# Kernel tuning notes

Measured on AMD Instinct MI355X. Metric: run time of the kernel, lower is better.

The kernel has to match this reference:

```python
import jax, jax.numpy as jnp
import numpy as np

UNITS = 1024
N_FEATURES = 128
OUT_STEPS = 32
EPS = 1e-7


def _lstm_cell(x, h, c, W, U, b):
    # Keras LSTMCell: gates ordered i, f, g(candidate), o
    z = x @ W + h @ U + b  # [B, 4U]
    i, f, g, o = jnp.split(z, 4, axis=-1)
    i = jax.nn.sigmoid(i)
    f = jax.nn.sigmoid(f)
    g = jnp.tanh(g)
    o = jax.nn.sigmoid(o)
    c_new = f * c + i * g
    h_new = o * jnp.tanh(c_new)
    return h_new, c_new


def setup_inputs() -> dict:
    key = jax.random.key(0)
    ks = jax.random.split(key, 12)
    B, T, F, U = 512, 64, N_FEATURES, UNITS
    s = lambda fan_in: 1.0 / np.sqrt(fan_in)
    return {
        "inputs": jax.random.normal(ks[0], (B, T, F), jnp.float32),
        "mean": jax.random.normal(ks[1], (F,), jnp.float32) * 0.1,
        "var": jax.random.uniform(ks[2], (F,), jnp.float32, 0.5, 1.5),
        "W1": jax.random.normal(ks[3], (F, 4 * U), jnp.float32) * s(F),
        "U1": jax.random.normal(ks[4], (U, 4 * U), jnp.float32) * s(U),
        "b1": jnp.zeros((4 * U,), jnp.float32),
        "W2": jax.random.normal(ks[5], (U, 4 * U), jnp.float32) * s(U),
        "U2": jax.random.normal(ks[6], (U, 4 * U), jnp.float32) * s(U),
        "b2": jnp.zeros((4 * U,), jnp.float32),
        "Wd": jax.random.normal(ks[7], (U, F), jnp.float32) * s(U),
        "bd": jnp.zeros((F,), jnp.float32),
    }


def reference(inputs, mean, var, W1, U1, b1, W2, U2, b2, Wd, bd):
    B = inputs.shape[0]
    inv_std = jax.lax.rsqrt(var + EPS)
    # NOTE: original call() normalizes, then warmup() normalizes AGAIN -- faithful.
    x = (inputs - mean) * inv_std
    x = (x - mean) * inv_std

    # --- warmup: RNN(cell1) over input sequence, return last h and state ---
    h0 = jnp.zeros((B, UNITS), x.dtype)
    c0 = jnp.zeros((B, UNITS), x.dtype)

    def warm_step(carry, xt):
        h, c = carry
        h, c = _lstm_cell(xt, h, c, W1, U1, b1)
        return (h, c), None

    (h, c), _ = jax.lax.scan(warm_step, (h0, c0), jnp.swapaxes(x, 0, 1))
    pred0 = h @ Wd + bd  # [B, F]

    def ar_step(carry, _):
        pred, h, c = carry
        h, c = _lstm_cell(pred, h, c, W1, U1, b1)
        h, c = _lstm_cell(h, h, c, W2, U2, b2)
        pred = h @ Wd + bd
        return (pred, h, c), pred

    _, preds = jax.lax.scan(ar_step, (pred0, h, c), None, length=OUT_STEPS - 1)
    preds = jnp.concatenate([pred0[None], preds], axis=0)  # [out_steps, B, F]
    return jnp.transpose(preds, (1, 0, 2))  # [B, out_steps, F]
```

## Files before the change

kernel.cpp:

```cpp
#include <hip/hip_runtime.h>
#include <stdint.h>

#define NB 512
#define NT 64
#define NF 128
#define NU 1024
#define NG 4096
#define NS 32

typedef __attribute__((ext_vector_type(8))) short short8;
typedef __attribute__((ext_vector_type(4))) float f32x4;
typedef __attribute__((ext_vector_type(16))) float f32x16;
typedef __attribute__((ext_vector_type(4))) unsigned int u32x4;

__device__ __forceinline__ float sigm(float x) { return 1.0f / (1.0f + __expf(-x)); }
__device__ __forceinline__ float tanh_f(float x) {
  float ax = fabsf(x);
  float e = __expf(2.0f * ax);
  float t = 1.0f - 2.0f / (e + 1.0f);
  return copysignf(t, x);
}
__device__ __forceinline__ unsigned short f2bf(float f) {
  union { float f; unsigned u; } v; v.f = f;
  unsigned r = v.u + 0x7fffu + ((v.u >> 16) & 1u);
  return (unsigned short)(r >> 16);
}

__device__ __forceinline__ void coh_store_bf16(unsigned short* p, unsigned v) {
  asm volatile("global_store_short %0, %1, off sc0 sc1" :: "v"(p), "v"(v) : "memory");
}

__device__ __forceinline__ void gbar_grp(unsigned* gf, int u_blk, unsigned gen) {
  __syncthreads();
  if (threadIdx.x == 0)
    __hip_atomic_store(gf + u_blk, gen, __ATOMIC_RELAXED, __HIP_MEMORY_SCOPE_AGENT);
  if (threadIdx.x < 32) {
    while (__hip_atomic_load(gf + threadIdx.x, __ATOMIC_RELAXED, __HIP_MEMORY_SCOPE_AGENT) < gen)
      __builtin_amdgcn_s_sleep(1);
  }
  __syncthreads();
}

template <int KX>
__device__ __forceinline__ void do_step(
    const unsigned short* __restrict__ hIn,
    const unsigned short* __restrict__ Bp,
    const unsigned short* __restrict__ Xp,
    const unsigned short* __restrict__ W1p,
    int tstep, f32x4 bA, f32x4& cst,
    unsigned short* __restrict__ hOut, unsigned short* __restrict__ hOut2,
    unsigned short* lds,
    int r0, int u0, int kh, int g, int tid)
{
  constexpr int ROWB = (NU + KX) * 2;
  const int lane = tid & 63;
  const int lu = lane & 31;
  const int lk = lane >> 5;

  {
    u32x4 ta[8], tb[8];
    int la[8], lb[8];
#pragma unroll
    for (int it = 0; it < 8; ++it) {
      int i = tid + it * 512;
      int r = i >> 7, cb = i & 127;
      la[it] = r * ROWB + ((cb * 16) ^ ((r & 7) << 4));
      const unsigned short* gp = hIn + (size_t)(r0 + r) * NU + cb * 8;
      asm volatile("global_load_dwordx4 %0, %1, off sc0 sc1" : "=v"(ta[it]) : "v"(gp));
    }
#pragma unroll
    for (int it = 0; it < 8; ++it) {
      int i = tid + (8 + it) * 512;
      int r = i >> 7, cb = i & 127;
      lb[it] = r * ROWB + ((cb * 16) ^ ((r & 7) << 4));
      const unsigned short* gp = hIn + (size_t)(r0 + r) * NU + cb * 8;
      asm volatile("global_load_dwordx4 %0, %1, off sc0 sc1" : "=v"(tb[it]) : "v"(gp));
    }
    if constexpr (KX > 0) {
      u32x4 tx[2]; int ox[2];
#pragma unroll
      for (int it = 0; it < 2; ++it) {
        int i = tid + it * 512;
        int r = i >> 4, cb = i & 15;
        ox[it] = r * ROWB + ((NU * 2 + cb * 16) ^ ((r & 7) << 4));
        const unsigned short* gp = Xp + ((size_t)tstep * NB + (r0 + r)) * NF + cb * 8;
        asm volatile("global_load_dwordx4 %0, %1, off" : "=v"(tx[it]) : "v"(gp));
      }
      asm volatile("s_waitcnt vmcnt(10)" ::: "memory");
      __builtin_amdgcn_sched_barrier(0);
#pragma unroll
      for (int it = 0; it < 8; ++it) *(u32x4*)((char*)lds + la[it]) = ta[it];
      asm volatile("s_waitcnt vmcnt(2)" ::: "memory");
      __builtin_amdgcn_sched_barrier(0);
#pragma unroll
      for (int it = 0; it < 8; ++it) *(u32x4*)((char*)lds + lb[it]) = tb[it];
      asm volatile("s_waitcnt vmcnt(0)" ::: "memory");
      __builtin_amdgcn_sched_barrier(0);
#pragma unroll
      for (int it = 0; it < 2; ++it) *(u32x4*)((char*)lds + ox[it]) = tx[it];
    } else {
      asm volatile("s_waitcnt vmcnt(8)" ::: "memory");
      __builtin_amdgcn_sched_barrier(0);
#pragma unroll
      for (int it = 0; it < 8; ++it) *(u32x4*)((char*)lds + la[it]) = ta[it];
      asm volatile("s_waitcnt vmcnt(0)" ::: "memory");
      __builtin_amdgcn_sched_barrier(0);
#pragma unroll
      for (int it = 0; it < 8; ++it) *(u32x4*)((char*)lds + lb[it]) = tb[it];
    }
  }
  __syncthreads();

  f32x16 acc0 = (f32x16)0.0f;
  f32x16 acc1 = (f32x16)0.0f;

  const char* ldsb = (const char*)lds;
  const int axor = (lane & 7) << 4;
  const int arow0 = lu * ROWB;
  const int arow1 = (32 + lu) * ROWB;
  const int kbase = kh * 1024;
  const size_t cB = (size_t)g * NU + u0 + lu;

  short8 nb0 = *(const short8*)(Bp + ((size_t)(kh * 64 + 0 + lk) * NG + cB) * 8);
  short8 nb1 = *(const short8*)(Bp + ((size_t)(kh * 64 + 2 + lk) * NG + cB) * 8);
#pragma unroll 4
  for (int kc = 0; kc < 32; ++kc) {
    short8 bb = (kc & 1) ? nb1 : nb0;
    if (kc < 30) {
      short8 nv = *(const short8*)(Bp + ((size_t)(kh * 64 + (kc + 2) * 2 + lk) * NG + cB) * 8);
      if (kc & 1) nb1 = nv; else nb0 = nv;
    }
    int kb = (kbase + kc * 32 + lk * 16) ^ axor;
    short8 a0 = *(const short8*)(ldsb + arow0 + kb);
    short8 a1 = *(const short8*)(ldsb + arow1 + kb);
    acc0 = __builtin_amdgcn_mfma_f32_32x32x16_bf16(a0, bb, acc0, 0, 0, 0);
    acc1 = __builtin_amdgcn_mfma_f32_32x32x16_bf16(a1, bb, acc1, 0, 0, 0);
  }
  if constexpr (KX > 0) {
#pragma unroll
    for (int kx = 0; kx < 4; ++kx) {
      short8 bb = *(const short8*)(W1p + ((size_t)(kh * 8 + kx * 2 + lk) * NG + cB) * 8);
      int kb = (NU * 2 + kh * 128 + kx * 32 + lk * 16) ^ axor;
      short8 a0 = *(const short8*)(ldsb + arow0 + kb);
      short8 a1 = *(const short8*)(ldsb + arow1 + kb);
      acc0 = __builtin_amdgcn_mfma_f32_32x32x16_bf16(a0, bb, acc0, 0, 0, 0);
      acc1 = __builtin_amdgcn_mfma_f32_32x32x16_bf16(a1, bb, acc1, 0, 0, 0);
    }
  }

  __syncthreads();
  float* ex = (float*)lds;
  const int w8 = kh * 4 + g;
#pragma unroll
  for (int e = 0; e < 16; ++e) {
    ex[(w8 * 2 + 0) * 1024 + e * 64 + lane] = acc0[e];
    ex[(w8 * 2 + 1) * 1024 + e * 64 + lane] = acc1[e];
  }
  __syncthreads();

  const int u = tid & 31;
  const int rb = (tid >> 5) << 2;
  const int rh = tid >> 8;
  const int c4 = (tid >> 6) & 3;
  const int lane_src = (((tid >> 5) & 1) << 5) | u;
  f32x4 z[4];
#pragma unroll
  for (int gg = 0; gg < 4; ++gg) {
#pragma unroll
    for (int j = 0; j < 4; ++j) {
      int e = c4 * 4 + j;
      z[gg][j] = ex[((0 + gg) * 2 + rh) * 1024 + e * 64 + lane_src]
               + ex[((4 + gg) * 2 + rh) * 1024 + e * 64 + lane_src];
    }
  }
#pragma unroll
  for (int j = 0; j < 4; ++j) {
    size_t idx = (size_t)(r0 + rb + j) * NU + (u0 + u);
    float iv = sigm(z[0][j] + bA[0]);
    float fv = sigm(z[1][j] + bA[1]);
    float gv = tanh_f(z[2][j] + bA[2]);
    float ov = sigm(z[3][j] + bA[3]);
    float cN = fv * cst[j] + iv * gv;
    cst[j] = cN;
    unsigned hv = f2bf(ov * tanh_f(cN));
    coh_store_bf16(hOut + idx, hv);
    if (hOut2) coh_store_bf16(hOut2 + idx, hv);
  }
}

__global__ __launch_bounds__(512, 1) void lstm_seq(
    const unsigned short* __restrict__ U1p, const unsigned short* __restrict__ U1pp,
    const unsigned short* __restrict__ W2U2p, const unsigned short* __restrict__ W1p,
    const unsigned short* __restrict__ x2,
    const float* __restrict__ b1, const float* __restrict__ b1p, const float* __restrict__ b2,
    unsigned short* __restrict__ h0, unsigned short* __restrict__ h1,
    unsigned short* __restrict__ hist, unsigned* __restrict__ flags)
{
  extern __shared__ unsigned short lds[];
  const int bid = blockIdx.x;
  const int xcd = bid & 7, slot = bid >> 3;
  const int u_blk = xcd * 4 + (slot >> 3);
  const int m_blk = slot & 7;
  const int r0 = m_blk * 64, u0 = u_blk * 32;
  const int tid = threadIdx.x;
  const int w = tid >> 6, kh = w >> 2, g = w & 3;
  const size_t HS = (size_t)NB * NU;
  unsigned* gf = flags + m_blk * 64;

  const int ub = u0 + (tid & 31);
  f32x4 bW, bC1, bC2;
#pragma unroll
  for (int gg = 0; gg < 4; ++gg) {
    bW[gg]  = b1 [gg * NU + ub];
    bC1[gg] = b1p[gg * NU + ub];
    bC2[gg] = b2 [gg * NU + ub];
  }
  f32x4 cst = (f32x4){0.f, 0.f, 0.f, 0.f};

  unsigned gen = 0;
  for (int t = 0; t < NT; ++t) {
    const unsigned short* hi = (t & 1) ? h1 : h0;
    unsigned short* ho = (t & 1) ? h0 : h1;
    do_step<NF>(hi, U1p, x2, W1p, t, bW, cst, ho, (t == NT - 1) ? hist : nullptr,
                lds, r0, u0, kh, g, tid);
    gbar_grp(gf, u_blk, ++gen);
  }
  for (int s = 0; s < NS - 1; ++s) {
    do_step<0>(h0, U1pp, nullptr, nullptr, 0, bC1, cst, h1, nullptr,
               lds, r0, u0, kh, g, tid);
    gbar_grp(gf, u_blk, ++gen);
    do_step<0>(h1, W2U2p, nullptr, nullptr, 0, bC2, cst, h0, hist + (size_t)(s + 1) * HS,
               lds, r0, u0, kh, g, tid);
    gbar_grp(gf, u_blk, ++gen);
  }
}

__global__ __launch_bounds__(256, 2) void pred_gemm(
    const unsigned short* __restrict__ H,
    const unsigned short* __restrict__ Wdp,
    const float* __restrict__ bd, float* __restrict__ out)
{
  __shared__ unsigned short lds[32 * NU];
  const int tid = threadIdx.x;
  const int r0 = blockIdx.x * 32;
  for (int i = tid; i < 32 * 128; i += 256) {
    int r = i >> 7, cb = i & 127;
    uint4 v = *(const uint4*)(H + (size_t)(r0 + r) * NU + cb * 8);
    int off = r * 2048 + ((cb * 16) ^ ((r & 7) << 4));
    *(uint4*)((char*)lds + off) = v;
  }
  __syncthreads();
  const int w = tid >> 6, l = tid & 63, lr = l & 15, g4 = l >> 4;
  f32x4 acc[2][2];
#pragma unroll
  for (int a = 0; a < 2; ++a)
#pragma unroll
    for (int c = 0; c < 2; ++c) acc[a][c] = (f32x4){0.f, 0.f, 0.f, 0.f};
  const char* ldsb = (const char*)lds;
  const int arow0 = lr * 2048, arow1 = (16 + lr) * 2048, axor = (lr & 7) << 4;
  const int col0 = w * 32 + lr;
#pragma unroll 4
  for (int kc = 0; kc < 32; ++kc) {
    int kb = (kc * 64 + g4 * 16) ^ axor;
    short8 a0 = *(const short8*)(ldsb + arow0 + kb);
    short8 a1 = *(const short8*)(ldsb + arow1 + kb);
    size_t base = ((size_t)(kc * 4 + g4) * NF) * 8;
    short8 w0 = *(const short8*)(Wdp + base + (size_t)col0 * 8);
    short8 w1 = *(const short8*)(Wdp + base + (size_t)(col0 + 16) * 8);
    acc[0][0] = __builtin_amdgcn_mfma_f32_16x16x32_bf16(a0, w0, acc[0][0], 0, 0, 0);
    acc[1][0] = __builtin_amdgcn_mfma_f32_16x16x32_bf16(a1, w0, acc[1][0], 0, 0, 0);
    acc[0][1] = __builtin_amdgcn_mfma_f32_16x16x32_bf16(a0, w1, acc[0][1], 0, 0, 0);
    acc[1][1] = __builtin_amdgcn_mfma_f32_16x16x32_bf16(a1, w1, acc[1][1], 0, 0, 0);
  }
#pragma unroll
  for (int rt = 0; rt < 2; ++rt)
#pragma unroll
    for (int ct = 0; ct < 2; ++ct)
#pragma unroll
      for (int j = 0; j < 4; ++j) {
        int r = r0 + rt * 16 + g4 * 4 + j;
        int s = r >> 9, bb = r & 511;
        int f = w * 32 + ct * 16 + lr;
        out[((size_t)bb * NS + s) * NF + f] = acc[rt][ct][j] + bd[f];
      }
}

__global__ void prep_x(const float* __restrict__ in, const float* __restrict__ mean,
                       const float* __restrict__ var, unsigned short* __restrict__ x2) {
  int i = (blockIdx.x * 256 + threadIdx.x) * 4;
  int f = i & 127;
  int bt = i >> 7;
  int b = bt >> 6, t = bt & 63;
  float4 v = *(const float4*)(in + i);
  float vv[4] = {v.x, v.y, v.z, v.w};
  unsigned short o[4] __attribute__((aligned(8)));
#pragma unroll
  for (int j = 0; j < 4; ++j) {
    float inv = rsqrtf(var[f + j] + 1e-7f);
    float s = inv * inv;
    float m2 = mean[f + j] * (s + inv);
    o[j] = f2bf(vv[j] * s - m2);
  }
  *(uint2*)(x2 + (((size_t)t * NB + b) << 7) + f) = *(const uint2*)o;
}

__global__ void prep_pack(const float* __restrict__ A, const float* __restrict__ A2,
                          unsigned short* __restrict__ P, int N) {
  int idx = blockIdx.x * 256 + threadIdx.x;
  int kg = idx / N, c = idx - kg * N;
  unsigned short o[8] __attribute__((aligned(16)));
#pragma unroll
  for (int j = 0; j < 8; ++j) {
    size_t e = (size_t)(kg * 8 + j) * N + c;
    float vv = A[e];
    if (A2) vv += A2[e];
    o[j] = f2bf(vv);
  }
  *(uint4*)(P + (size_t)idx * 8) = *(const uint4*)o;
}

__global__ __launch_bounds__(256) void prep_u1pp(
    const float* __restrict__ U1, const float* __restrict__ Wd,
    const float* __restrict__ W1, unsigned short* __restrict__ P) {
  __shared__ float wd[8][NF];
  const int kg = blockIdx.x >> 4;
  const int c = ((blockIdx.x & 15) << 8) + threadIdx.x;
  for (int i = threadIdx.x; i < 8 * NF; i += 256)
    wd[i >> 7][i & 127] = Wd[(size_t)(kg * 8 + (i >> 7)) * NF + (i & 127)];
  __syncthreads();
  float a[8];
#pragma unroll
  for (int j = 0; j < 8; ++j) a[j] = U1[(size_t)(kg * 8 + j) * NG + c];
#pragma unroll 8
  for (int m = 0; m < NF; ++m) {
    float w1v = W1[(size_t)m * NG + c];
#pragma unroll
    for (int j = 0; j < 8; ++j) a[j] += wd[j][m] * w1v;
  }
  unsigned short o[8] __attribute__((aligned(16)));
#pragma unroll
  for (int j = 0; j < 8; ++j) o[j] = f2bf(a[j]);
  *(uint4*)(P + (size_t)(kg * NG + c) * 8) = *(const uint4*)o;
}

__global__ void prep_wdp(const float* __restrict__ Wd, unsigned short* __restrict__ P) {
  int idx = blockIdx.x * 256 + threadIdx.x;
  int kg = idx >> 7, f = idx & 127;
  unsigned short o[8] __attribute__((aligned(16)));
#pragma unroll
  for (int j = 0; j < 8; ++j) o[j] = f2bf(Wd[(size_t)(kg * 8 + j) * NF + f]);
  *(uint4*)(P + (size_t)idx * 8) = *(const uint4*)o;
}

__global__ void prep_b1p(const float* __restrict__ b1, const float* __restrict__ bd,
                         const float* __restrict__ W1, float* __restrict__ o) {
  int c = blockIdx.x * 256 + threadIdx.x;
  float acc = b1[c];
#pragma unroll 8
  for (int m = 0; m < NF; ++m) acc += bd[m] * W1[(size_t)m * NG + c];
  o[c] = acc;
}

extern "C" void kernel_launch(void* const* d_in, const int* in_sizes, int n_in,
                              void* d_out, int out_size, void* d_ws, size_t ws_size,
                              hipStream_t stream) {
  const float* inputs = (const float*)d_in[0];
  const float* mean = (const float*)d_in[1];
  const float* var  = (const float*)d_in[2];
  const float* W1   = (const float*)d_in[3];
  const float* U1   = (const float*)d_in[4];
  const float* b1   = (const float*)d_in[5];
  const float* W2   = (const float*)d_in[6];
  const float* U2   = (const float*)d_in[7];
  const float* b2   = (const float*)d_in[8];
  const float* Wd   = (const float*)d_in[9];
  const float* bd   = (const float*)d_in[10];
  float* out = (float*)d_out;
  char* ws = (char*)d_ws;

  size_t off = 0;
  auto alloc = [&](size_t bytes) { char* p = ws + off; off += (bytes + 255) & ~255ull; return p; };
  unsigned short* h0    = (unsigned short*)alloc((size_t)NB * NU * 2);
  unsigned short* h1    = (unsigned short*)alloc((size_t)NB * NU * 2);
  unsigned short* hist  = (unsigned short*)alloc((size_t)NS * NB * NU * 2);
  unsigned short* x2    = (unsigned short*)alloc((size_t)NB * NT * NF * 2);
  unsigned short* U1p   = (unsigned short*)alloc((size_t)NU * NG * 2);
  unsigned short* U1pp  = (unsigned short*)alloc((size_t)NU * NG * 2);
  unsigned short* W2U2p = (unsigned short*)alloc((size_t)NU * NG * 2);
  unsigned short* W1p   = (unsigned short*)alloc((size_t)NF * NG * 2);
  unsigned short* Wdp   = (unsigned short*)alloc((size_t)NU * NF * 2);
  float* b1p            = (float*)alloc((size_t)NG * 4);
  unsigned* flags       = (unsigned*)alloc(8 * 64 * 4);

  hipMemsetAsync(h0, 0, (size_t)NB * NU * 2, stream);
  hipMemsetAsync(flags, 0, 8 * 64 * 4, stream);

  prep_x   <<<(NB * NT * NF) / 1024, 256, 0, stream>>>(inputs, mean, var, x2);
  prep_pack<<<(NU / 8) * NG / 256, 256, 0, stream>>>(U1, nullptr, U1p, NG);
  prep_u1pp<<<(NU / 8) * NG / 256, 256, 0, stream>>>(U1, Wd, W1, U1pp);
  prep_pack<<<(NU / 8) * NG / 256, 256, 0, stream>>>(W2, U2, W2U2p, NG);
  prep_pack<<<(NF / 8) * NG / 256, 256, 0, stream>>>(W1, nullptr, W1p, NG);
  prep_wdp <<<(NU / 8) * NF / 256, 256, 0, stream>>>(Wd, Wdp);
  prep_b1p <<<NG / 256, 256, 0, stream>>>(b1, bd, W1, b1p);

  lstm_seq<<<256, 512, 64 * (NU + NF) * 2, stream>>>(U1p, U1pp, W2U2p, W1p, x2,
                                                     b1, b1p, b2, h0, h1, hist, flags);

  pred_gemm<<<(NS * NB) / 32, 256, 0, stream>>>(hist, Wdp, bd, out);
}
```

Before: 1.198 ms.

## Double LSTM block to 1024 threads, splitting row halves across waves

Each persistent LSTM block now runs 16 waves instead of 8. Each wave handles one 32-row half of the 64-row tile with a single MFMA accumulator instead of two, and the h-tile loads, LDS exchange and gate epilogue are re-indexed so every thread handles 2 rows instead of 4. The aim is to shorten the serial per-step latency through more parallelism and MFMA issue slots. In exchange, each B-operand weight fragment is now loaded by two waves instead of one, and the larger block adds barrier overhead and register pressure.

Result: slower. 1.358 ms (+13.3%).

```diff
diff --git a/kernel.cpp b/kernel.cpp
--- a/kernel.cpp
+++ b/kernel.cpp
@@ -50,7 +50,7 @@
     int tstep, f32x4 bA, f32x4& cst,
     unsigned short* __restrict__ hOut, unsigned short* __restrict__ hOut2,
     unsigned short* lds,
-    int r0, int u0, int kh, int g, int tid)
+    int r0, int u0, int rh, int kh, int g, int tid)
 {
   constexpr int ROWB = (NU + KX) * 2;
   const int lane = tid & 63;
@@ -58,66 +58,53 @@
   const int lk = lane >> 5;
 
   {
-    u32x4 ta[8], tb[8];
-    int la[8], lb[8];
+    u32x4 t[8];
+    int lo[8];
 #pragma unroll
     for (int it = 0; it < 8; ++it) {
-      int i = tid + it * 512;
+      int i = tid + it * 1024;
       int r = i >> 7, cb = i & 127;
-      la[it] = r * ROWB + ((cb * 16) ^ ((r & 7) << 4));
+      lo[it] = r * ROWB + ((cb * 16) ^ ((r & 7) << 4));
       const unsigned short* gp = hIn + (size_t)(r0 + r) * NU + cb * 8;
-      asm volatile("global_load_dwordx4 %0, %1, off sc0 sc1" : "=v"(ta[it]) : "v"(gp));
-    }
-#pragma unroll
-    for (int it = 0; it < 8; ++it) {
-      int i = tid + (8 + it) * 512;
-      int r = i >> 7, cb = i & 127;
-      lb[it] = r * ROWB + ((cb * 16) ^ ((r & 7) << 4));
-      const unsigned short* gp = hIn + (size_t)(r0 + r) * NU + cb * 8;
-      asm volatile("global_load_dwordx4 %0, %1, off sc0 sc1" : "=v"(tb[it]) : "v"(gp));
+      asm volatile("global_load_dwordx4 %0, %1, off sc0 sc1" : "=v"(t[it]) : "v"(gp));
     }
     if constexpr (KX > 0) {
-      u32x4 tx[2]; int ox[2];
-#pragma unroll
-      for (int it = 0; it < 2; ++it) {
-        int i = tid + it * 512;
-        int r = i >> 4, cb = i & 15;
-        ox[it] = r * ROWB + ((NU * 2 + cb * 16) ^ ((r & 7) << 4));
+      u32x4 tx; int ox;
+      {
+        int r = tid >> 4, cb = tid & 15;
+        ox = r * ROWB + ((NU * 2 + cb * 16) ^ ((r & 7) << 4));
         const unsigned short* gp = Xp + ((size_t)tstep * NB + (r0 + r)) * NF + cb * 8;
-        asm volatile("global_load_dwordx4 %0, %1, off" : "=v"(tx[it]) : "v"(gp));
+        asm volatile("global_load_dwordx4 %0, %1, off" : "=v"(tx) : "v"(gp));
       }
-      asm volatile("s_waitcnt vmcnt(10)" ::: "memory");
-      __builtin_amdgcn_sched_barrier(0);
-#pragma unroll
-      for (int it = 0; it < 8; ++it) *(u32x4*)((char*)lds + la[it]) = ta[it];
-      asm volatile("s_waitcnt vmcnt(2)" ::: "memory");
-      __builtin_amdgcn_sched_barrier(0);
-#pragma unroll
-      for (int it = 0; it < 8; ++it) *(u32x4*)((char*)lds + lb[it]) = tb[it];
+      asm volatile("s_waitcnt vmcnt(5)" ::: "memory");
+      __builtin_amdgcn_sched_barrier(0);
+#pragma unroll
+      for (int it = 0; it < 4; ++it) *(u32x4*)((char*)lds + lo[it]) = t[it];
+      asm volatile("s_waitcnt vmcnt(1)" ::: "memory");
+      __builtin_amdgcn_sched_barrier(0);
+#pragma unroll
+      for (int it = 4; it < 8; ++it) *(u32x4*)((char*)lds + lo[it]) = t[it];
       asm volatile("s_waitcnt vmcnt(0)" ::: "memory");
       __builtin_amdgcn_sched_barrier(0);
-#pragma unroll
-      for (int it = 0; it < 2; ++it) *(u32x4*)((char*)lds + ox[it]) = tx[it];
+      *(u32x4*)((char*)lds + ox) = tx;
     } else {
-      asm volatile("s_waitcnt vmcnt(8)" ::: "memory");
-      __builtin_amdgcn_sched_barrier(0);
-#pragma unroll
-      for (int it = 0; it < 8; ++it) *(u32x4*)((char*)lds + la[it]) = ta[it];
+      asm volatile("s_waitcnt vmcnt(4)" ::: "memory");
+      __builtin_amdgcn_sched_barrier(0);
+#pragma unroll
+      for (int it = 0; it < 4; ++it) *(u32x4*)((char*)lds + lo[it]) = t[it];
       asm volatile("s_waitcnt vmcnt(0)" ::: "memory");
       __builtin_amdgcn_sched_barrier(0);
 #pragma unroll
-      for (int it = 0; it < 8; ++it) *(u32x4*)((char*)lds + lb[it]) = tb[it];
+      for (int it = 4; it < 8; ++it) *(u32x4*)((char*)lds + lo[it]) = t[it];
     }
   }
   __syncthreads();
 
-  f32x16 acc0 = (f32x16)0.0f;
-  f32x16 acc1 = (f32x16)0.0f;
+  f32x16 acc = (f32x16)0.0f;
 
   const char* ldsb = (const char*)lds;
   const int axor = (lane & 7) << 4;
-  const int arow0 = lu * ROWB;
-  const int arow1 = (32 + lu) * ROWB;
+  const int arow = (rh * 32 + lu) * ROWB;
   const int kbase = kh * 1024;
   const size_t cB = (size_t)g * NU + u0 + lu;
 
@@ -131,64 +118,54 @@
       if (kc & 1) nb1 = nv; else nb0 = nv;
     }
     int kb = (kbase + kc * 32 + lk * 16) ^ axor;
-    short8 a0 = *(const short8*)(ldsb + arow0 + kb);
-    short8 a1 = *(const short8*)(ldsb + arow1 + kb);
-    acc0 = __builtin_amdgcn_mfma_f32_32x32x16_bf16(a0, bb, acc0, 0, 0, 0);
-    acc1 = __builtin_amdgcn_mfma_f32_32x32x16_bf16(a1, bb, acc1, 0, 0, 0);
+    short8 a = *(const short8*)(ldsb + arow + kb);
+    acc = __builtin_amdgcn_mfma_f32_32x32x16_bf16(a, bb, acc, 0, 0, 0);
   }
   if constexpr (KX > 0) {
 #pragma unroll
     for (int kx = 0; kx < 4; ++kx) {
       short8 bb = *(const short8*)(W1p + ((size_t)(kh * 8 + kx * 2 + lk) * NG + cB) * 8);
       int kb = (NU * 2 + kh * 128 + kx * 32 + lk * 16) ^ axor;
-      short8 a0 = *(const short8*)(ldsb + arow0 + kb);
-      short8 a1 = *(const short8*)(ldsb + arow1 + kb);
-      acc0 = __builtin_amdgcn_mfma_f32_32x32x16_bf16(a0, bb, acc0, 0, 0, 0);
-      acc1 = __builtin_amdgcn_mfma_f32_32x32x16_bf16(a1, bb, acc1, 0, 0, 0);
+      short8 a = *(const short8*)(ldsb + arow + kb);
+      acc = __builtin_amdgcn_mfma_f32_32x32x16_bf16(a, bb, acc, 0, 0, 0);
     }
   }
 
   __syncthreads();
   float* ex = (float*)lds;
-  const int w8 = kh * 4 + g;
-#pragma unroll
-  for (int e = 0; e < 16; ++e) {
-    ex[(w8 * 2 + 0) * 1024 + e * 64 + lane] = acc0[e];
-    ex[(w8 * 2 + 1) * 1024 + e * 64 + lane] = acc1[e];
-  }
+  const int w16 = (rh << 3) | (kh << 2) | g;
+#pragma unroll
+  for (int e = 0; e < 16; ++e)
+    ex[w16 * 1024 + e * 64 + lane] = acc[e];
   __syncthreads();
 
   const int u = tid & 31;
-  const int rb = (tid >> 5) << 2;
-  const int rh = tid >> 8;
-  const int c4 = (tid >> 6) & 3;
-  const int lane_src = (((tid >> 5) & 1) << 5) | u;
-  f32x4 z[4];
-#pragma unroll
-  for (int gg = 0; gg < 4; ++gg) {
-#pragma unroll
-    for (int j = 0; j < 4; ++j) {
-      int e = c4 * 4 + j;
-      z[gg][j] = ex[((0 + gg) * 2 + rh) * 1024 + e * 64 + lane_src]
-               + ex[((4 + gg) * 2 + rh) * 1024 + e * 64 + lane_src];
-    }
-  }
-#pragma unroll
-  for (int j = 0; j < 4; ++j) {
-    size_t idx = (size_t)(r0 + rb + j) * NU + (u0 + u);
-    float iv = sigm(z[0][j] + bA[0]);
-    float fv = sigm(z[1][j] + bA[1]);
-    float gv = tanh_f(z[2][j] + bA[2]);
-    float ov = sigm(z[3][j] + bA[3]);
-    float cN = fv * cst[j] + iv * gv;
-    cst[j] = cN;
+  const int rr = tid >> 5;
+#pragma unroll
+  for (int rj = 0; rj < 2; ++rj) {
+    int r = rr * 2 + rj;
+    int rh2 = r >> 5, rl = r & 31;
+    int lane_src = (((rl >> 2) & 1) << 5) | u;
+    int e = (rl & 3) + ((rl >> 3) << 2);
+    float zz[4];
+#pragma unroll
+    for (int gg = 0; gg < 4; ++gg)
+      zz[gg] = ex[(size_t)(((rh2 << 3) | gg) * 1024) + e * 64 + lane_src]
+             + ex[(size_t)(((rh2 << 3) | 4 | gg) * 1024) + e * 64 + lane_src];
+    float iv = sigm(zz[0] + bA[0]);
+    float fv = sigm(zz[1] + bA[1]);
+    float gv = tanh_f(zz[2] + bA[2]);
+    float ov = sigm(zz[3] + bA[3]);
+    float cN = fv * cst[rj] + iv * gv;
+    cst[rj] = cN;
     unsigned hv = f2bf(ov * tanh_f(cN));
+    size_t idx = (size_t)(r0 + r) * NU + (u0 + u);
     coh_store_bf16(hOut + idx, hv);
     if (hOut2) coh_store_bf16(hOut2 + idx, hv);
   }
 }
 
-__global__ __launch_bounds__(512, 1) void lstm_seq(
+__global__ __launch_bounds__(1024, 1) void lstm_seq(
     const unsigned short* __restrict__ U1p, const unsigned short* __restrict__ U1pp,
     const unsigned short* __restrict__ W2U2p, const unsigned short* __restrict__ W1p,
     const unsigned short* __restrict__ x2,
@@ -203,7 +180,8 @@
   const int m_blk = slot & 7;
   const int r0 = m_blk * 64, u0 = u_blk * 32;
   const int tid = threadIdx.x;
-  const int w = tid >> 6, kh = w >> 2, g = w & 3;
+  const int w = tid >> 6;
+  const int rh = w >> 3, kh = (w >> 2) & 1, g = w & 3;
   const size_t HS = (size_t)NB * NU;
   unsigned* gf = flags + m_blk * 64;
 
@@ -222,15 +200,15 @@
     const unsigned short* hi = (t & 1) ? h1 : h0;
     unsigned short* ho = (t & 1) ? h0 : h1;
     do_step<NF>(hi, U1p, x2, W1p, t, bW, cst, ho, (t == NT - 1) ? hist : nullptr,
-                lds, r0, u0, kh, g, tid);
+                lds, r0, u0, rh, kh, g, tid);
     gbar_grp(gf, u_blk, ++gen);
   }
   for (int s = 0; s < NS - 1; ++s) {
     do_step<0>(h0, U1pp, nullptr, nullptr, 0, bC1, cst, h1, nullptr,
-               lds, r0, u0, kh, g, tid);
+               lds, r0, u0, rh, kh, g, tid);
     gbar_grp(gf, u_blk, ++gen);
     do_step<0>(h1, W2U2p, nullptr, nullptr, 0, bC2, cst, h0, hist + (size_t)(s + 1) * HS,
-               lds, r0, u0, kh, g, tid);
+               lds, r0, u0, rh, kh, g, tid);
     gbar_grp(gf, u_blk, ++gen);
   }
 }
@@ -403,8 +381,8 @@
   prep_wdp <<<(NU / 8) * NF / 256, 256, 0, stream>>>(Wd, Wdp);
   prep_b1p <<<NG / 256, 256, 0, stream>>>(b1, bd, W1, b1p);
 
-  lstm_seq<<<256, 512, 64 * (NU + NF) * 2, stream>>>(U1p, U1pp, W2U2p, W1p, x2,
-                                                     b1, b1p, b2, h0, h1, hist, flags);
+  lstm_seq<<<256, 1024, 64 * (NU + NF) * 2, stream>>>(U1p, U1pp, W2U2p, W1p, x2,
+                                                      b1, b1p, b2, h0, h1, hist, flags);
 
   pred_gemm<<<(NS * NB) / 32, 256, 0, stream>>>(hist, Wdp, bd, out);
 }
```
